# Kernel optimization log

Hardware: AMD Instinct MI355X
Metric: run time of the kernel (lower is better)

## Reference

```python
import jax, jax.numpy as jnp
import numpy as np

N_NODES = 4096
IN_FEAT = 256
N_HEADS = 8
N_HIDDEN = 32  # out_features // n_heads
NEG_SLOPE = 0.2


def setup_inputs() -> dict:
    key = jax.random.key(0)
    k1, k2, k3, k4 = jax.random.split(key, 4)
    h = jax.random.normal(k1, (N_NODES, IN_FEAT), dtype=jnp.float32)
    W = jax.random.normal(k2, (N_HEADS * N_HIDDEN, IN_FEAT), dtype=jnp.float32) * 0.05
    a = jax.random.normal(k3, (2 * N_HIDDEN,), dtype=jnp.float32) * 0.05
    adj_mat = jax.random.randint(k4, (N_NODES, N_NODES, 1), 0, 2, dtype=jnp.int32)
    return {"h": h, "W": W, "a": a, "adj_mat": adj_mat}


def reference(h, W, a, adj_mat):
    n = h.shape[0]
    # g = linear(h) -> [N, H, F]
    g = (h @ W.T).reshape(n, N_HEADS, N_HIDDEN)
    # e_ij = LeakyReLU(a^T [g_i || g_j]) = LeakyReLU(a_l . g_i + a_r . g_j)
    a_l, a_r = a[:N_HIDDEN], a[N_HIDDEN:]
    s_i = jnp.einsum('nhf,f->nh', g, a_l)  # destination term (repeat_interleave axis)
    s_j = jnp.einsum('nhf,f->nh', g, a_r)  # source term (repeat axis)
    e = jax.nn.leaky_relu(s_i[:, None, :] + s_j[None, :, :], NEG_SLOPE)  # [N, N, H]
    e = jnp.where(adj_mat == 0, jnp.float32(-jnp.inf), e)
    att = jax.nn.softmax(e, axis=1)  # softmax over source nodes j
    # dropout(p) in eval mode -> identity
    out = jnp.einsum('ijh,jhf->ihf', att, g)
    return out.reshape(n, N_HEADS * N_HIDDEN)  # is_concat=True
```

## Files before the change

kernel.cpp:

```cpp
#include <hip/hip_runtime.h>
#include <math.h>

constexpr int N   = 4096;
constexpr int F   = 256;
constexpr int NH  = 8;
constexpr int HID = 32;
constexpr float SLOPE = 0.2f;

using h2       = __attribute__((ext_vector_type(2))) _Float16;
using frag_f16 = __attribute__((ext_vector_type(8))) _Float16;
using frag_cd  = __attribute__((ext_vector_type(4))) float;
using frag_c16 = __attribute__((ext_vector_type(16))) float;

__device__ inline unsigned short f2h(float x) {
  _Float16 v = (_Float16)x;
  unsigned short u; __builtin_memcpy(&u, &v, 2); return u;
}

__global__ __launch_bounds__(256) void k_pre(const float* __restrict__ h,
                                             const float* __restrict__ W,
                                             const float* __restrict__ a,
                                             const int* __restrict__ adj,
                                             unsigned short* __restrict__ hb,
                                             float* __restrict__ U,
                                             unsigned int* __restrict__ bits,
                                             float* __restrict__ outp,
                                             float* __restrict__ lbuf) {
  const int b = blockIdx.x, t = threadIdx.x;
  if (b < 544) {
    const int idx8 = (b * 256 + t) * 8;
    const float* src = (idx8 < N * F) ? (h + idx8) : (W + idx8 - N * F);
    const float4 v0 = *(const float4*)src;
    const float4 v1 = *(const float4*)(src + 4);
    unsigned short tmp[8];
    tmp[0] = f2h(v0.x); tmp[1] = f2h(v0.y); tmp[2] = f2h(v0.z); tmp[3] = f2h(v0.w);
    tmp[4] = f2h(v1.x); tmp[5] = f2h(v1.y); tmp[6] = f2h(v1.z); tmp[7] = f2h(v1.w);
    *(int4*)(hb + idx8) = *(int4*)tmp;
  } else if (b < 560) {
    const int c = b - 544, k = t;
    const int head = c & 7, side = c >> 3;
    float acc = 0.f;
#pragma unroll
    for (int f = 0; f < 32; ++f)
      acc += W[(size_t)(head * 32 + f) * F + k] * a[side * 32 + f];
    U[c * F + k] = acc;
  } else if (b < 2608) {
    const int lane = t & 63, w = t >> 6;
    const int row  = (b - 560) * 2 + (w >> 1);
    const int half = w & 1;
    const int4* arow = (const int4*)(adj + (size_t)row * N) + half * 512;
    unsigned int* brow = bits + (size_t)row * (N / 32) + half * 64;
#pragma unroll
    for (int c = 0; c < 8; ++c) {
      const int4 av = arow[c * 64 + lane];
      unsigned int v = (av.x != 0 ? 1u : 0u) | (av.y != 0 ? 2u : 0u) |
                       (av.z != 0 ? 4u : 0u) | (av.w != 0 ? 8u : 0u);
      v <<= ((lane & 7) * 4);
      v |= __shfl_xor(v, 1);
      v |= __shfl_xor(v, 2);
      v |= __shfl_xor(v, 4);
      if ((lane & 7) == 0) brow[c * 8 + (lane >> 3)] = v;
    }
  } else if (b < 2864) {
    const int base = (b - 2608) * 256 + t;
#pragma unroll
    for (int q = 0; q < 4; ++q)
      *(float4*)(outp + ((size_t)q * 65536 + base) * 4) =
          make_float4(0.f, 0.f, 0.f, 0.f);
  } else {
    *(float4*)(lbuf + ((size_t)(b - 2864) * 256 + t) * 4) =
        make_float4(0.f, 0.f, 0.f, 0.f);
  }
}

__global__ __launch_bounds__(256) void k_mid(const float* __restrict__ h,
                                             const float* __restrict__ U,
                                             const unsigned short* __restrict__ hb,
                                             const unsigned short* __restrict__ Wb,
                                             unsigned int* __restrict__ RT2,
                                             unsigned short* __restrict__ BT,
                                             unsigned short* __restrict__ DT,
                                             unsigned short* __restrict__ gT) {
  __shared__ float hs[16][260];
  __shared__ float Us[16][260];
  const int b = blockIdx.x, t = threadIdx.x;
  if (b < 256) {
    const int i0 = b * 16;
    {
      const int r = t >> 4, s0 = (t & 15) * 16;
      const float4* src = (const float4*)(h + (size_t)(i0 + r) * F + s0);
      const float4* usr = (const float4*)(U + (size_t)r * F + s0);
#pragma unroll
      for (int q = 0; q < 4; ++q) {
        *(float4*)&hs[r][s0 + q * 4] = src[q];
        *(float4*)&Us[r][s0 + q * 4] = usr[q];
      }
    }
    __syncthreads();
    const int r = t >> 4, c = t & 15;
    float acc = 0.f;
#pragma unroll
    for (int k4 = 0; k4 < 64; ++k4) {
      const float4 hv = *(const float4*)&hs[r][k4 * 4];
      const float4 uv = *(const float4*)&Us[c][k4 * 4];
      acc += hv.x * uv.x + hv.y * uv.y + hv.z * uv.z + hv.w * uv.w;
    }
    const int n = i0 + r;
    if (c < 8) {
      const unsigned int r16 = f2h(__expf(-0.8f * acc));
      RT2[(size_t)n * NH + c] = (r16 << 16) | r16;
    } else {
      const int hd = c - 8;
      BT[(size_t)hd * N + n] = f2h(__expf(acc));
      DT[(size_t)hd * N + n] = f2h(__expf(SLOPE * acc));
    }
  } else {
    const int lane = t & 63;
    const int tile = (b - 256) * 4 + (t >> 6);
    const int mt = tile >> 4, nt = tile & 15;
    const int m0 = mt * 16, n0 = nt * 16;
    const int n16 = lane & 15, quad = lane >> 4;
    frag_cd acc = {0.f, 0.f, 0.f, 0.f};
    const unsigned short* ap = hb + (size_t)(m0 + n16) * F + quad * 8;
    const unsigned short* bp = Wb + (size_t)(n0 + n16) * F + quad * 8;
#pragma unroll
    for (int ks = 0; ks < F / 32; ++ks) {
      const frag_f16 af = *(const frag_f16*)(ap + ks * 32);
      const frag_f16 bf = *(const frag_f16*)(bp + ks * 32);
      acc = __builtin_amdgcn_mfma_f32_16x16x32_f16(af, bf, acc, 0, 0, 0);
    }
    unsigned short tmp[4];
#pragma unroll
    for (int reg = 0; reg < 4; ++reg) tmp[reg] = f2h(acc[reg]);
    *(int2*)(gT + (size_t)(n0 + n16) * N + m0 + quad * 4) = *(int2*)tmp;
  }
}

constexpr int TI = 32;
constexpr int NSPLIT = 4;

__global__ __launch_bounds__(256, 6) void k_agg(
    const unsigned short* __restrict__ gT,
    const unsigned int* __restrict__ RT2,
    const unsigned short* __restrict__ BT, const unsigned short* __restrict__ DT,
    const unsigned int* __restrict__ bits,
    float* __restrict__ outp, float* __restrict__ lbuf) {
  __shared__ __align__(16) unsigned short sB[64][140];
  __shared__ float sMl[2][32];

  const int t    = threadIdx.x;
  const int lane = t & 63;
  const int wv   = t >> 6;
  const int hd   = wv >> 1;
  const int jh   = wv & 1;
  const int b    = blockIdx.x;
  const int hp   = b & 3;
  const int js   = (b >> 2) & (NSPLIT - 1);
  const int i0   = (b >> 4) * TI;
  const int head = hp * 2 + hd;

  const int n32 = lane & 31;
  const int kh  = lane >> 5;
  const int shmb = jh * 16 + kh * 8;

  const int myi = i0 + n32;
  const unsigned int Ri2u = RT2[(size_t)myi * NH + head];
  h2 Ri2; __builtin_memcpy(&Ri2, &Ri2u, 4);
  const uint4* bp4 = (const uint4*)(bits + (size_t)myi * (N / 32) + js * 32);

  const unsigned short* BTh = BT + (size_t)head * N + js * 1024;
  const unsigned short* DTh = DT + (size_t)head * N + js * 1024;

  frag_c16 acc = {0.f, 0.f, 0.f, 0.f, 0.f, 0.f, 0.f, 0.f,
                  0.f, 0.f, 0.f, 0.f, 0.f, 0.f, 0.f, 0.f};
  float lpart = 0.f;
#if __has_builtin(__builtin_amdgcn_fdot2)
  const h2 one2 = {(_Float16)1.0f, (_Float16)1.0f};
#endif

  const int sr = t >> 2, ss0 = t & 3;
  const unsigned short* gsrc = gT + (size_t)(hp * 64 + sr) * N + js * 1024;

  for (int c8 = 0; c8 < 8; ++c8) {
    __syncthreads();
    {
#pragma unroll
      for (int s = 0; s < 4; ++s) {
        const int seg = ss0 + s * 4;
        const int4 v = *(const int4*)(gsrc + c8 * 128 + seg * 8);
        *(int2*)&sB[sr][seg * 8]     = make_int2(v.x, v.y);
        *(int2*)&sB[sr][seg * 8 + 4] = make_int2(v.z, v.w);
      }
    }
    uint4 Bv[4], Dv[4];
#pragma unroll
    for (int sh = 0; sh < 4; ++sh) {
      const int jb = (sh * 2 + jh) * 16 + kh * 8;
      Bv[sh] = *(const uint4*)(BTh + c8 * 128 + jb);
      Dv[sh] = *(const uint4*)(DTh + c8 * 128 + jb);
    }
    const uint4 bw = bp4[c8];
    const unsigned int bwa[4] = {bw.x, bw.y, bw.z, bw.w};
    __syncthreads();
#pragma unroll
    for (int sh = 0; sh < 4; ++sh) {
      const int jb = (sh * 2 + jh) * 16 + kh * 8;
      const unsigned int mb = (bwa[sh] >> shmb) & 0xFFu;
      const unsigned int bu[4] = {Bv[sh].x, Bv[sh].y, Bv[sh].z, Bv[sh].w};
      const unsigned int du[4] = {Dv[sh].x, Dv[sh].y, Dv[sh].z, Dv[sh].w};
      unsigned int packed[4];
#pragma unroll
      for (int p = 0; p < 4; ++p) {
        h2 hB, hD;
        __builtin_memcpy(&hB, &bu[p], 4);
        __builtin_memcpy(&hD, &du[p], 4);
        const h2 wm = __builtin_elementwise_max(hB, Ri2 * hD);
        unsigned int wp; __builtin_memcpy(&wp, &wm, 4);
        const unsigned int d  = (mb >> (2 * p)) & 3u;
        const unsigned int sp = ((d | (d << 15)) & 0x10001u) * 0xFFFFu;
        wp &= sp;
        packed[p] = wp;
        h2 wh; __builtin_memcpy(&wh, &wp, 4);
#if __has_builtin(__builtin_amdgcn_fdot2)
        lpart = __builtin_amdgcn_fdot2(wh, one2, lpart, false);
#else
        lpart += (float)wh.x + (float)wh.y;
#endif
      }
      frag_f16 af; __builtin_memcpy(&af, packed, 16);

      const int frow = hd * 32 + n32;
      const int2 blo = *(const int2*)&sB[frow][jb];
      const int2 bhi = *(const int2*)&sB[frow][jb + 4];
      const int bt[4] = {blo.x, blo.y, bhi.x, bhi.y};
      frag_f16 bf; __builtin_memcpy(&bf, bt, 16);

      acc = __builtin_amdgcn_mfma_f32_32x32x16_f16(af, bf, acc, 0, 0, 0);
    }
  }

  float* mrg = (float*)&sB[0][0];
  const float lp2 = lpart + __shfl_xor(lpart, 32);
  __syncthreads();
  if (jh == 1) {
#pragma unroll
    for (int reg = 0; reg < 16; ++reg) {
      const int row = (reg & 3) + 8 * (reg >> 2) + 4 * kh;
      mrg[(size_t)(hd * 32 + row) * 32 + n32] = acc[reg];
    }
    if (kh == 0) sMl[hd][n32] = lp2;
  }
  __syncthreads();
  if (jh == 0) {
    const float lt = lp2 + sMl[hd][n32];
    if (kh == 0) atomicAdd(&lbuf[(size_t)(i0 + n32) * NH + head], lt);
#pragma unroll
    for (int reg = 0; reg < 16; ++reg) {
      const int row = (reg & 3) + 8 * (reg >> 2) + 4 * kh;
      const float v = acc[reg] + mrg[(size_t)(hd * 32 + row) * 32 + n32];
      atomicAdd(&outp[(size_t)(i0 + row) * F + head * HID + n32], v);
    }
  }
}

__global__ __launch_bounds__(256) void k_norm(float* __restrict__ outp,
                                              const float* __restrict__ lbuf) {
  const int idx = blockIdx.x * 256 + threadIdx.x;
  const int i = idx >> 6, fq = idx & 63;
  const int hh = fq >> 3;
  const float inv = 1.f / lbuf[(size_t)i * NH + hh];
  float4 v = *(float4*)(outp + (size_t)idx * 4);
  v.x *= inv; v.y *= inv; v.z *= inv; v.w *= inv;
  *(float4*)(outp + (size_t)idx * 4) = v;
}

extern "C" void kernel_launch(void* const* d_in, const int* in_sizes, int n_in,
                              void* d_out, int out_size, void* d_ws, size_t ws_size,
                              hipStream_t stream) {
  const float* h   = (const float*)d_in[0];
  const float* W   = (const float*)d_in[1];
  const float* a   = (const float*)d_in[2];
  const int*   adj = (const int*)d_in[3];
  float* out = (float*)d_out;

  char* ws = (char*)d_ws;
  unsigned short* hb = (unsigned short*)ws;  ws += (size_t)(N * F + F * F) * 2;
  unsigned short* Wb = hb + (size_t)N * F;
  unsigned short* gT = (unsigned short*)ws;  ws += (size_t)N * F * 2;
  unsigned int* bits = (unsigned int*)ws;    ws += (size_t)N * (N / 32) * 4;
  float* U    = (float*)ws;                  ws += 16 * F * 4;
  unsigned int* RT2 = (unsigned int*)ws;     ws += (size_t)N * NH * 4;
  unsigned short* BT = (unsigned short*)ws;  ws += (size_t)N * NH * 2;
  unsigned short* DT = (unsigned short*)ws;  ws += (size_t)N * NH * 2;
  float* lbuf = (float*)ws;                  ws += (size_t)N * NH * 4;

  k_pre<<<dim3(2896), dim3(256), 0, stream>>>(h, W, a, adj, hb, U, bits, out, lbuf);
  k_mid<<<dim3(1280), dim3(256), 0, stream>>>(h, U, hb, Wb, RT2, BT, DT, gT);
  k_agg<<<dim3((N / TI) * 4 * NSPLIT), dim3(256), 0, stream>>>(
      gT, RT2, BT, DT, bits, out, lbuf);
  k_norm<<<dim3(N * F / 4 / 256), dim3(256), 0, stream>>>(out, lbuf);
}
```

Before: 157.5 us.

## Merge pre/mid kernels and restructure aggregation with larger i-tile and prefetch

Merges the conversion, U-projection, score and projection GEMM stages into one front kernel. The score blocks now recompute U redundantly per block, and the GEMM converts fp32 to fp16 on the fly, removing the hb/Wb/U intermediates and one launch. The aggregation kernel moves from 32 to 64 destination rows per block, with each wave owning 32 rows and sweeping all j, so the shared-memory cross-wave merge goes away. It also adds register prefetch of the next gT chunk into shared memory. In exchange, every score block recomputes U, which adds global reads of W, and occupancy drops to 4 blocks per CU.

```diff
diff --git a/kernel.cpp b/kernel.cpp
--- a/kernel.cpp
+++ b/kernel.cpp
@@ -17,36 +17,85 @@
   unsigned short u; __builtin_memcpy(&u, &v, 2); return u;
 }
 
-__global__ __launch_bounds__(256) void k_pre(const float* __restrict__ h,
-                                             const float* __restrict__ W,
-                                             const float* __restrict__ a,
-                                             const int* __restrict__ adj,
-                                             unsigned short* __restrict__ hb,
-                                             float* __restrict__ U,
-                                             unsigned int* __restrict__ bits,
-                                             float* __restrict__ outp,
-                                             float* __restrict__ lbuf) {
+__global__ __launch_bounds__(256) void k_front(const float* __restrict__ h,
+                                               const float* __restrict__ W,
+                                               const float* __restrict__ a,
+                                               const int* __restrict__ adj,
+                                               unsigned int* __restrict__ RT2,
+                                               unsigned short* __restrict__ BT,
+                                               unsigned short* __restrict__ DT,
+                                               unsigned short* __restrict__ gT,
+                                               unsigned int* __restrict__ bits,
+                                               float* __restrict__ outp,
+                                               float* __restrict__ lbuf) {
+  __shared__ float hs[16][260];
+  __shared__ float Us[16][260];
   const int b = blockIdx.x, t = threadIdx.x;
-  if (b < 544) {
-    const int idx8 = (b * 256 + t) * 8;
-    const float* src = (idx8 < N * F) ? (h + idx8) : (W + idx8 - N * F);
-    const float4 v0 = *(const float4*)src;
-    const float4 v1 = *(const float4*)(src + 4);
-    unsigned short tmp[8];
-    tmp[0] = f2h(v0.x); tmp[1] = f2h(v0.y); tmp[2] = f2h(v0.z); tmp[3] = f2h(v0.w);
-    tmp[4] = f2h(v1.x); tmp[5] = f2h(v1.y); tmp[6] = f2h(v1.z); tmp[7] = f2h(v1.w);
-    *(int4*)(hb + idx8) = *(int4*)tmp;
-  } else if (b < 560) {
-    const int c = b - 544, k = t;
-    const int head = c & 7, side = c >> 3;
+  if (b < 256) {
+    const int i0 = b * 16;
+    {
+      const int r = t >> 4, s0 = (t & 15) * 16;
+      const float4* src = (const float4*)(h + (size_t)(i0 + r) * F + s0);
+#pragma unroll
+      for (int q = 0; q < 4; ++q) *(float4*)&hs[r][s0 + q * 4] = src[q];
+    }
+    {
+      const int k = t;
+      for (int c = 0; c < 16; ++c) {
+        const int head = c & 7, side = c >> 3;
+        float acc = 0.f;
+#pragma unroll
+        for (int f = 0; f < 32; ++f)
+          acc += W[(size_t)(head * 32 + f) * F + k] * a[side * 32 + f];
+        Us[c][k] = acc;
+      }
+    }
+    __syncthreads();
+    const int r = t >> 4, c = t & 15;
     float acc = 0.f;
 #pragma unroll
-    for (int f = 0; f < 32; ++f)
-      acc += W[(size_t)(head * 32 + f) * F + k] * a[side * 32 + f];
-    U[c * F + k] = acc;
-  } else if (b < 2608) {
+    for (int k4 = 0; k4 < 64; ++k4) {
+      const float4 hv = *(const float4*)&hs[r][k4 * 4];
+      const float4 uv = *(const float4*)&Us[c][k4 * 4];
+      acc += hv.x * uv.x + hv.y * uv.y + hv.z * uv.z + hv.w * uv.w;
+    }
+    const int n = i0 + r;
+    if (c < 8) {
+      const unsigned int r16 = f2h(__expf(-0.8f * acc));
+      RT2[(size_t)n * NH + c] = (r16 << 16) | r16;
+    } else {
+      const int hd = c - 8;
+      BT[(size_t)hd * N + n] = f2h(__expf(acc));
+      DT[(size_t)hd * N + n] = f2h(__expf(SLOPE * acc));
+    }
+  } else if (b < 1280) {
+    const int lane = t & 63;
+    const int tile = (b - 256) * 4 + (t >> 6);
+    const int mt = tile >> 4, nt = tile & 15;
+    const int m0 = mt * 16, n0 = nt * 16;
+    const int n16 = lane & 15, quad = lane >> 4;
+    frag_cd acc = {0.f, 0.f, 0.f, 0.f};
+    const float* ap = h + (size_t)(m0 + n16) * F + quad * 8;
+    const float* bp = W + (size_t)(n0 + n16) * F + quad * 8;
+#pragma unroll
+    for (int ks = 0; ks < F / 32; ++ks) {
+      const float4 a0 = *(const float4*)(ap + ks * 32);
+      const float4 a1 = *(const float4*)(ap + ks * 32 + 4);
+      const float4 b0 = *(const float4*)(bp + ks * 32);
+      const float4 b1 = *(const float4*)(bp + ks * 32 + 4);
+      const frag_f16 af = {(_Float16)a0.x, (_Float16)a0.y, (_Float16)a0.z, (_Float16)a0.w,
+                           (_Float16)a1.x, (_Float16)a1.y, (_Float16)a1.z, (_Float16)a1.w};
+      const frag_f16 bf = {(_Float16)b0.x, (_Float16)b0.y, (_Float16)b0.z, (_Float16)b0.w,
+                           (_Float16)b1.x, (_Float16)b1.y, (_Float16)b1.z, (_Float16)b1.w};
+      acc = __builtin_amdgcn_mfma_f32_16x16x32_f16(af, bf, acc, 0, 0, 0);
+    }
+    unsigned short tmp[4];
+#pragma unroll
+    for (int reg = 0; reg < 4; ++reg) tmp[reg] = f2h(acc[reg]);
+    *(int2*)(gT + (size_t)(n0 + n16) * N + m0 + quad * 4) = *(int2*)tmp;
+  } else if (b < 3328) {
     const int lane = t & 63, w = t >> 6;
-    const int row  = (b - 560) * 2 + (w >> 1);
+    const int row  = (b - 1280) * 2 + (w >> 1);
     const int half = w & 1;
     const int4* arow = (const int4*)(adj + (size_t)row * N) + half * 512;
     unsigned int* brow = bits + (size_t)row * (N / 32) + half * 64;
@@ -61,98 +110,34 @@
       v |= __shfl_xor(v, 4);
       if ((lane & 7) == 0) brow[c * 8 + (lane >> 3)] = v;
     }
-  } else if (b < 2864) {
-    const int base = (b - 2608) * 256 + t;
+  } else if (b < 3584) {
+    const int base = (b - 3328) * 256 + t;
 #pragma unroll
     for (int q = 0; q < 4; ++q)
       *(float4*)(outp + ((size_t)q * 65536 + base) * 4) =
           make_float4(0.f, 0.f, 0.f, 0.f);
   } else {
-    *(float4*)(lbuf + ((size_t)(b - 2864) * 256 + t) * 4) =
+    *(float4*)(lbuf + ((size_t)(b - 3584) * 256 + t) * 4) =
         make_float4(0.f, 0.f, 0.f, 0.f);
   }
 }
 
-__global__ __launch_bounds__(256) void k_mid(const float* __restrict__ h,
-                                             const float* __restrict__ U,
-                                             const unsigned short* __restrict__ hb,
-                                             const unsigned short* __restrict__ Wb,
-                                             unsigned int* __restrict__ RT2,
-                                             unsigned short* __restrict__ BT,
-                                             unsigned short* __restrict__ DT,
-                                             unsigned short* __restrict__ gT) {
-  __shared__ float hs[16][260];
-  __shared__ float Us[16][260];
-  const int b = blockIdx.x, t = threadIdx.x;
-  if (b < 256) {
-    const int i0 = b * 16;
-    {
-      const int r = t >> 4, s0 = (t & 15) * 16;
-      const float4* src = (const float4*)(h + (size_t)(i0 + r) * F + s0);
-      const float4* usr = (const float4*)(U + (size_t)r * F + s0);
-#pragma unroll
-      for (int q = 0; q < 4; ++q) {
-        *(float4*)&hs[r][s0 + q * 4] = src[q];
-        *(float4*)&Us[r][s0 + q * 4] = usr[q];
-      }
-    }
-    __syncthreads();
-    const int r = t >> 4, c = t & 15;
-    float acc = 0.f;
-#pragma unroll
-    for (int k4 = 0; k4 < 64; ++k4) {
-      const float4 hv = *(const float4*)&hs[r][k4 * 4];
-      const float4 uv = *(const float4*)&Us[c][k4 * 4];
-      acc += hv.x * uv.x + hv.y * uv.y + hv.z * uv.z + hv.w * uv.w;
-    }
-    const int n = i0 + r;
-    if (c < 8) {
-      const unsigned int r16 = f2h(__expf(-0.8f * acc));
-      RT2[(size_t)n * NH + c] = (r16 << 16) | r16;
-    } else {
-      const int hd = c - 8;
-      BT[(size_t)hd * N + n] = f2h(__expf(acc));
-      DT[(size_t)hd * N + n] = f2h(__expf(SLOPE * acc));
-    }
-  } else {
-    const int lane = t & 63;
-    const int tile = (b - 256) * 4 + (t >> 6);
-    const int mt = tile >> 4, nt = tile & 15;
-    const int m0 = mt * 16, n0 = nt * 16;
-    const int n16 = lane & 15, quad = lane >> 4;
-    frag_cd acc = {0.f, 0.f, 0.f, 0.f};
-    const unsigned short* ap = hb + (size_t)(m0 + n16) * F + quad * 8;
-    const unsigned short* bp = Wb + (size_t)(n0 + n16) * F + quad * 8;
-#pragma unroll
-    for (int ks = 0; ks < F / 32; ++ks) {
-      const frag_f16 af = *(const frag_f16*)(ap + ks * 32);
-      const frag_f16 bf = *(const frag_f16*)(bp + ks * 32);
-      acc = __builtin_amdgcn_mfma_f32_16x16x32_f16(af, bf, acc, 0, 0, 0);
-    }
-    unsigned short tmp[4];
-#pragma unroll
-    for (int reg = 0; reg < 4; ++reg) tmp[reg] = f2h(acc[reg]);
-    *(int2*)(gT + (size_t)(n0 + n16) * N + m0 + quad * 4) = *(int2*)tmp;
-  }
-}
-
-constexpr int TI = 32;
+constexpr int TI = 64;
 constexpr int NSPLIT = 4;
 
-__global__ __launch_bounds__(256, 6) void k_agg(
+__global__ __launch_bounds__(256, 4) void k_agg(
     const unsigned short* __restrict__ gT,
     const unsigned int* __restrict__ RT2,
     const unsigned short* __restrict__ BT, const unsigned short* __restrict__ DT,
     const unsigned int* __restrict__ bits,
     float* __restrict__ outp, float* __restrict__ lbuf) {
   __shared__ __align__(16) unsigned short sB[64][140];
-  __shared__ float sMl[2][32];
 
   const int t    = threadIdx.x;
   const int lane = t & 63;
   const int wv   = t >> 6;
+  const int isub = wv & 1;
   const int hd   = wv >> 1;
-  const int jh   = wv & 1;
   const int b    = blockIdx.x;
   const int hp   = b & 3;
   const int js   = (b >> 2) & (NSPLIT - 1);
@@ -161,9 +146,8 @@
 
   const int n32 = lane & 31;
   const int kh  = lane >> 5;
-  const int shmb = jh * 16 + kh * 8;
-
-  const int myi = i0 + n32;
+
+  const int myi = i0 + isub * 32 + n32;
   const unsigned int Ri2u = RT2[(size_t)myi * NH + head];
   h2 Ri2; __builtin_memcpy(&Ri2, &Ri2u, 4);
   const uint4* bp4 = (const uint4*)(bits + (size_t)myi * (N / 32) + js * 32);
@@ -181,33 +165,37 @@
   const int sr = t >> 2, ss0 = t & 3;
   const unsigned short* gsrc = gT + (size_t)(hp * 64 + sr) * N + js * 1024;
 
+  {
+    int4 pre[4];
+#pragma unroll
+    for (int s = 0; s < 4; ++s)
+      pre[s] = *(const int4*)(gsrc + (ss0 + s * 4) * 8);
+#pragma unroll
+    for (int s = 0; s < 4; ++s) {
+      const int seg = ss0 + s * 4;
+      *(int2*)&sB[sr][seg * 8]     = make_int2(pre[s].x, pre[s].y);
+      *(int2*)&sB[sr][seg * 8 + 4] = make_int2(pre[s].z, pre[s].w);
+    }
+  }
+  __syncthreads();
+
   for (int c8 = 0; c8 < 8; ++c8) {
-    __syncthreads();
-    {
-#pragma unroll
-      for (int s = 0; s < 4; ++s) {
-        const int seg = ss0 + s * 4;
-        const int4 v = *(const int4*)(gsrc + c8 * 128 + seg * 8);
-        *(int2*)&sB[sr][seg * 8]     = make_int2(v.x, v.y);
-        *(int2*)&sB[sr][seg * 8 + 4] = make_int2(v.z, v.w);
-      }
-    }
-    uint4 Bv[4], Dv[4];
-#pragma unroll
-    for (int sh = 0; sh < 4; ++sh) {
-      const int jb = (sh * 2 + jh) * 16 + kh * 8;
-      Bv[sh] = *(const uint4*)(BTh + c8 * 128 + jb);
-      Dv[sh] = *(const uint4*)(DTh + c8 * 128 + jb);
+    int4 nxt[4];
+    if (c8 < 7) {
+#pragma unroll
+      for (int s = 0; s < 4; ++s)
+        nxt[s] = *(const int4*)(gsrc + (c8 + 1) * 128 + (ss0 + s * 4) * 8);
     }
     const uint4 bw = bp4[c8];
     const unsigned int bwa[4] = {bw.x, bw.y, bw.z, bw.w};
-    __syncthreads();
-#pragma unroll
-    for (int sh = 0; sh < 4; ++sh) {
-      const int jb = (sh * 2 + jh) * 16 + kh * 8;
-      const unsigned int mb = (bwa[sh] >> shmb) & 0xFFu;
-      const unsigned int bu[4] = {Bv[sh].x, Bv[sh].y, Bv[sh].z, Bv[sh].w};
-      const unsigned int du[4] = {Dv[sh].x, Dv[sh].y, Dv[sh].z, Dv[sh].w};
+#pragma unroll
+    for (int ss = 0; ss < 8; ++ss) {
+      const int jb = ss * 16 + kh * 8;
+      const uint4 Bv = *(const uint4*)(BTh + c8 * 128 + jb);
+      const uint4 Dv = *(const uint4*)(DTh + c8 * 128 + jb);
+      const unsigned int mb = (bwa[ss >> 1] >> (((ss & 1) << 4) + (kh << 3))) & 0xFFu;
+      const unsigned int bu[4] = {Bv.x, Bv.y, Bv.z, Bv.w};
+      const unsigned int du[4] = {Dv.x, Dv.y, Dv.z, Dv.w};
       unsigned int packed[4];
 #pragma unroll
       for (int p = 0; p < 4; ++p) {
@@ -237,29 +225,24 @@
 
       acc = __builtin_amdgcn_mfma_f32_32x32x16_f16(af, bf, acc, 0, 0, 0);
     }
-  }
-
-  float* mrg = (float*)&sB[0][0];
+    if (c8 < 7) {
+      __syncthreads();
+#pragma unroll
+      for (int s = 0; s < 4; ++s) {
+        const int seg = ss0 + s * 4;
+        *(int2*)&sB[sr][seg * 8]     = make_int2(nxt[s].x, nxt[s].y);
+        *(int2*)&sB[sr][seg * 8 + 4] = make_int2(nxt[s].z, nxt[s].w);
+      }
+      __syncthreads();
+    }
+  }
+
   const float lp2 = lpart + __shfl_xor(lpart, 32);
-  __syncthreads();
-  if (jh == 1) {
-#pragma unroll
-    for (int reg = 0; reg < 16; ++reg) {
-      const int row = (reg & 3) + 8 * (reg >> 2) + 4 * kh;
-      mrg[(size_t)(hd * 32 + row) * 32 + n32] = acc[reg];
-    }
-    if (kh == 0) sMl[hd][n32] = lp2;
-  }
-  __syncthreads();
-  if (jh == 0) {
-    const float lt = lp2 + sMl[hd][n32];
-    if (kh == 0) atomicAdd(&lbuf[(size_t)(i0 + n32) * NH + head], lt);
-#pragma unroll
-    for (int reg = 0; reg < 16; ++reg) {
-      const int row = (reg & 3) + 8 * (reg >> 2) + 4 * kh;
-      const float v = acc[reg] + mrg[(size_t)(hd * 32 + row) * 32 + n32];
-      atomicAdd(&outp[(size_t)(i0 + row) * F + head * HID + n32], v);
-    }
+  if (kh == 0) atomicAdd(&lbuf[(size_t)myi * NH + head], lp2);
+#pragma unroll
+  for (int reg = 0; reg < 16; ++reg) {
+    const int row = (reg & 3) + 8 * (reg >> 2) + 4 * kh;
+    atomicAdd(&outp[(size_t)(i0 + isub * 32 + row) * F + head * HID + n32], acc[reg]);
   }
 }
 
@@ -284,18 +267,15 @@
   float* out = (float*)d_out;
 
   char* ws = (char*)d_ws;
-  unsigned short* hb = (unsigned short*)ws;  ws += (size_t)(N * F + F * F) * 2;
-  unsigned short* Wb = hb + (size_t)N * F;
   unsigned short* gT = (unsigned short*)ws;  ws += (size_t)N * F * 2;
   unsigned int* bits = (unsigned int*)ws;    ws += (size_t)N * (N / 32) * 4;
-  float* U    = (float*)ws;                  ws += 16 * F * 4;
   unsigned int* RT2 = (unsigned int*)ws;     ws += (size_t)N * NH * 4;
   unsigned short* BT = (unsigned short*)ws;  ws += (size_t)N * NH * 2;
   unsigned short* DT = (unsigned short*)ws;  ws += (size_t)N * NH * 2;
   float* lbuf = (float*)ws;                  ws += (size_t)N * NH * 4;
 
-  k_pre<<<dim3(2896), dim3(256), 0, stream>>>(h, W, a, adj, hb, U, bits, out, lbuf);
-  k_mid<<<dim3(1280), dim3(256), 0, stream>>>(h, U, hb, Wb, RT2, BT, DT, gT);
+  k_front<<<dim3(3616), dim3(256), 0, stream>>>(h, W, a, adj, RT2, BT, DT, gT,
+                                                bits, out, lbuf);
   k_agg<<<dim3((N / TI) * 4 * NSPLIT), dim3(256), 0, stream>>>(
       gT, RT2, BT, DT, bits, out, lbuf);
   k_norm<<<dim3(N * F / 4 / 256), dim3(256), 0, stream>>>(out, lbuf);
```

New measurement: 161.9 us. +2.7%, slower.
